# Kernel optimization log

Measured on AMD Instinct MI355X. Metric: run time of the kernel, lower is better.

The kernel has to match this reference:

```python
import jax, jax.numpy as jnp
import numpy as np

B, T, D, H, L, OUT = 512, 82, 129, 1024, 2, 128
TOTAL_LEN = 182  # decoder runs TOTAL_LEN - T = 100 steps


def setup_inputs() -> dict:
    key = jax.random.key(0)
    ks = jax.random.split(key, 32)
    s = 1.0 / np.sqrt(H)  # torch LSTM default init scale
    def p(k, shape):
        return jax.random.uniform(k, shape, dtype=jnp.float32, minval=-s, maxval=s)
    inp = {}
    inp["x"] = jax.random.normal(ks[0], (B, T, D), dtype=jnp.float32)
    inp["lengths"] = jax.random.randint(ks[1], (B,), 1, T + 1, dtype=jnp.int32)
    idx = 2
    for pre, in0 in (("enc", D), ("dec", D - 1)):
        dims = [in0, H]
        for l in range(L):
            inp[f"{pre}_Wih{l}"] = p(ks[idx], (4 * H, dims[l])); idx += 1
            inp[f"{pre}_Whh{l}"] = p(ks[idx], (4 * H, H)); idx += 1
            inp[f"{pre}_bih{l}"] = p(ks[idx], (4 * H,)); idx += 1
            inp[f"{pre}_bhh{l}"] = p(ks[idx], (4 * H,)); idx += 1
    inp["fc_W"] = p(ks[idx], (OUT, H)); idx += 1
    inp["fc_b"] = p(ks[idx], (OUT,))
    return inp


def _cell(x, h, c, Wih, Whh, bih, bhh):
    # torch gate order: i, f, g, o
    g = x @ Wih.T + h @ Whh.T + (bih + bhh)
    i, f, gg, o = jnp.split(g, 4, axis=-1)
    c_new = jax.nn.sigmoid(f) * c + jax.nn.sigmoid(i) * jnp.tanh(gg)
    h_new = jax.nn.sigmoid(o) * jnp.tanh(c_new)
    return h_new, c_new


def _forward(x, lengths, enc, dec, fc_W, fc_b):
    Bsz, Tlen, _ = x.shape
    h0 = jnp.zeros((L, Bsz, H), x.dtype)
    c0 = jnp.zeros((L, Bsz, H), x.dtype)
    xs = jnp.swapaxes(x, 0, 1)  # [T, B, D]
    # packed-sequence semantics: state frozen once t >= lengths[b]
    mask = (jnp.arange(Tlen)[:, None] < lengths[None, :])[..., None]  # [T, B, 1]

    def enc_step(carry, inp):
        h, c = carry
        xt, m = inp
        layer_in = xt
        hs, cs = [], []
        for l in range(L):
            hn, cn = _cell(layer_in, h[l], c[l], *enc[l])
            hn = jnp.where(m, hn, h[l])
            cn = jnp.where(m, cn, c[l])
            hs.append(hn); cs.append(cn)
            layer_in = hn
        return (jnp.stack(hs), jnp.stack(cs)), None

    (h, c), _ = jax.lax.scan(enc_step, (h0, c0), (xs, mask))

    steps = TOTAL_LEN - Tlen
    x0 = jnp.zeros((Bsz, D - 1), x.dtype)

    def dec_step(carry, _):
        h, c, xt = carry
        layer_in = xt
        hs, cs = [], []
        for l in range(L):
            hn, cn = _cell(layer_in, h[l], c[l], *dec[l])
            hs.append(hn); cs.append(cn)
            layer_in = hn
        out = layer_in @ fc_W.T + fc_b  # [B, OUT]
        return (jnp.stack(hs), jnp.stack(cs), out), out

    _, outs = jax.lax.scan(dec_step, (h, c, x0), None, length=steps)
    return jnp.swapaxes(outs, 0, 1)  # [B, steps, OUT]


def reference(x, lengths,
              enc_Wih0, enc_Whh0, enc_bih0, enc_bhh0,
              enc_Wih1, enc_Whh1, enc_bih1, enc_bhh1,
              dec_Wih0, dec_Whh0, dec_bih0, dec_bhh0,
              dec_Wih1, dec_Whh1, dec_bih1, dec_bhh1,
              fc_W, fc_b):
    enc = [(enc_Wih0, enc_Whh0, enc_bih0, enc_bhh0),
           (enc_Wih1, enc_Whh1, enc_bih1, enc_bhh1)]
    dec = [(dec_Wih0, dec_Whh0, dec_bih0, dec_bhh0),
           (dec_Wih1, dec_Whh1, dec_bih1, dec_bhh1)]
    return _forward(x, lengths, enc, dec, fc_W, fc_b)
```

## Files before the change

### kernel.cpp

```cpp
#include <hip/hip_runtime.h>
#include <stdint.h>

#define BB 512
#define TT 82
#define DD 129
#define DXP 192
#define HH 1024
#define G4 4096
#define NOUT 128
#define NSTEPS 100

typedef unsigned short u16;
typedef __attribute__((ext_vector_type(8))) _Float16 f16x8;
typedef __attribute__((ext_vector_type(8))) short short8;
typedef __attribute__((ext_vector_type(4))) float f32x4;

__device__ __forceinline__ u16 f2h(float f) {
  _Float16 h = (_Float16)f;
  return __builtin_bit_cast(u16, h);
}
__device__ __forceinline__ float sigm(float x) { return 1.f / (1.f + __expf(-x)); }
__device__ __forceinline__ float tanhfast(float x) {
  float ax = fabsf(x);
  float e = __expf(2.f * ax);
  float t = 1.f - 2.f / (e + 1.f);
  return copysignf(t, x);
}
__device__ __forceinline__ void glds16(const void* g, void* l) {
  __builtin_amdgcn_global_load_lds((const __attribute__((address_space(1))) void*)g,
                                   (__attribute__((address_space(3))) void*)l, 16, 0, 0);
}

struct GemmP {
  const u16* A0; const u16* W0; const u16* A1; const u16* W1;
  const float* bias; float* cst; u16* hnext;
  int K0, K1, t;
  float* scratch; int mode;
};

template <int FUSE>
__global__ __launch_bounds__(256) void step_gemm(
    GemmP q0, GemmP q1, const int* __restrict__ lengths, float* __restrict__ fout)
{
  const GemmP p = (blockIdx.z == 0) ? q0 : q1;
  __shared__ __align__(16) u16 At[2][64 * 64];
  __shared__ __align__(16) u16 Bt[2][64 * 64];
  const int tid = threadIdx.x;
  const int lane = tid & 63;
  const int w = tid >> 6;
  const int m0 = blockIdx.y * 64;
  const int n0 = blockIdx.x * 64;

  const int nIter0 = p.K0 >> 6;
  const int nIterT = nIter0 + (p.K1 >> 6);

  auto stage = [&](int i, int buf) {
    const u16* A; const u16* W; int K; int kb;
    if (i < nIter0) { A = p.A0; W = p.W0; K = p.K0; kb = i << 6; }
    else            { A = p.A1; W = p.W1; K = p.K1; kb = (i - nIter0) << 6; }
    #pragma unroll
    for (int j = 0; j < 2; ++j) {
      int slot = tid + j * 256;
      int r = slot >> 3, c = slot & 7;
      int g = c ^ (r & 7);
      glds16(A + (size_t)(m0 + r) * K + kb + g * 8,
             &At[buf][(j * 256 + w * 64) * 8]);
    }
    #pragma unroll
    for (int j = 0; j < 2; ++j) {
      int slot = tid + j * 256;
      int r = slot >> 3, c = slot & 7;
      int g = c ^ (r & 7);
      glds16(W + (size_t)(n0 + r) * K + kb + g * 8,
             &Bt[buf][(j * 256 + w * 64) * 8]);
    }
  };

  f32x4 acc[4] = {};

  stage(0, 0);
  for (int i = 0; i < nIterT; ++i) {
    __syncthreads();
    if (i + 1 < nIterT) stage(i + 1, (i + 1) & 1);
    const int buf = i & 1;
    #pragma unroll
    for (int kc = 0; kc < 2; ++kc) {
      f16x8 af, bfr[4];
      const int gch = kc * 4 + (lane >> 4);
      {
        int r = w * 16 + (lane & 15);
        int c = gch ^ (r & 7);
        af = __builtin_bit_cast(f16x8, *(const short8*)&At[buf][(r * 8 + c) * 8]);
      }
      #pragma unroll
      for (int tj = 0; tj < 4; ++tj) {
        int r = tj * 16 + (lane & 15);
        int c = gch ^ (r & 7);
        bfr[tj] = __builtin_bit_cast(f16x8, *(const short8*)&Bt[buf][(r * 8 + c) * 8]);
      }
      #pragma unroll
      for (int tj = 0; tj < 4; ++tj)
        acc[tj] = __builtin_amdgcn_mfma_f32_16x16x32_f16(af, bfr[tj], acc[tj], 0, 0, 0);
    }
  }
  __syncthreads();

  const int col = lane & 15;
  const int rq = (lane >> 4) << 2;

  if (FUSE == 1) {
    const int mb = m0 + w * 16 + rq;
    if (p.mode == 2) {
      #pragma unroll
      for (int tj = 0; tj < 4; ++tj) {
        const int n = n0 + tj * 16 + col;
        #pragma unroll
        for (int r = 0; r < 4; ++r)
          p.scratch[((size_t)(mb + r) << 12) + n] = acc[tj][r];
      }
    } else {
      const int j = blockIdx.x * 16 + col;
      float bv[4];
      #pragma unroll
      for (int tj = 0; tj < 4; ++tj) bv[tj] = p.bias[n0 + tj * 16 + col];
      #pragma unroll
      for (int r = 0; r < 4; ++r) {
        const int m = mb + r;
        const size_t idx = ((size_t)m << 10) + j;
        const bool upd = (p.t < 0) || (p.t < lengths[m]);
        if (upd) {
          float g[4];
          #pragma unroll
          for (int tj = 0; tj < 4; ++tj) g[tj] = acc[tj][r] + bv[tj];
          if (p.mode == 1) {
            #pragma unroll
            for (int tj = 0; tj < 4; ++tj)
              g[tj] += p.scratch[((size_t)m << 12) + n0 + tj * 16 + col];
          }
          float cv = p.cst[idx];
          float cn = sigm(g[1]) * cv + sigm(g[0]) * tanhfast(g[2]);
          float hn = sigm(g[3]) * tanhfast(cn);
          p.cst[idx] = cn;
          p.hnext[idx] = f2h(hn);
        } else {
          p.hnext[idx] = p.A0[idx];
        }
      }
    }
  } else {
    const int mb = m0 + w * 16 + rq;
    #pragma unroll
    for (int tj = 0; tj < 4; ++tj) {
      const int n = n0 + tj * 16 + col;
      const float bv = p.bias[n];
      #pragma unroll
      for (int r = 0; r < 4; ++r) {
        const int m = mb + r;
        const float v = acc[tj][r] + bv;
        if (FUSE == 0) {
          fout[(size_t)m * (NSTEPS * NOUT) + n] = v;
        } else {
          fout[((size_t)(m & (BB - 1)) * NSTEPS + (m >> 9)) * NOUT + n] = v;
        }
      }
    }
  }
}

__global__ void conv_wp(const float* __restrict__ w, u16* __restrict__ wb,
                        int C, int Cp, int R, int perm, int total)
{
  int idx = blockIdx.x * 256 + threadIdx.x;
  if (idx >= total) return;
  int cc = idx % Cp;
  int n = idx / Cp;
  int orig = perm ? (((n >> 4) & 3) * (R >> 2) + (n >> 6) * 16 + (n & 15)) : n;
  wb[idx] = f2h(cc < C ? w[(size_t)orig * C + cc] : 0.f);
}

__global__ void conv_b(const float* __restrict__ b1, const float* __restrict__ b2,
                       float* __restrict__ bp)
{
  int n = blockIdx.x * 256 + threadIdx.x;
  if (n >= G4) return;
  int orig = ((n >> 4) & 3) * HH + (n >> 6) * 16 + (n & 15);
  bp[n] = b1[orig] + b2[orig];
}

__global__ void weff_kernel(const float* __restrict__ wih0, const float* __restrict__ fcW,
                            u16* __restrict__ weffb)
{
  int idx = blockIdx.x * 256 + threadIdx.x;
  int k = idx & (HH - 1);
  int n = idx >> 10;
  int orig = ((n >> 4) & 3) * HH + (n >> 6) * 16 + (n & 15);
  float s = 0.f;
  #pragma unroll 4
  for (int j = 0; j < NOUT; ++j) s += wih0[orig * NOUT + j] * fcW[(size_t)j * HH + k];
  weffb[idx] = f2h(s);
}

__global__ void beff_kernel(const float* __restrict__ bih, const float* __restrict__ bhh,
                            const float* __restrict__ wih0, const float* __restrict__ fcb,
                            float* __restrict__ bp)
{
  int n = blockIdx.x * 256 + threadIdx.x;
  if (n >= G4) return;
  int orig = ((n >> 4) & 3) * HH + (n >> 6) * 16 + (n & 15);
  float s = bih[orig] + bhh[orig];
  #pragma unroll 4
  for (int j = 0; j < NOUT; ++j) s += wih0[orig * NOUT + j] * fcb[j];
  bp[n] = s;
}

__global__ void conv_x(const float* __restrict__ x, u16* __restrict__ xb)
{
  int idx = blockIdx.x * 256 + threadIdx.x;
  if (idx >= TT * BB * DXP) return;
  int k = idx % DXP;
  int tb = idx / DXP;
  int b = tb & (BB - 1);
  int t = tb / BB;
  xb[idx] = f2h(k < DD ? x[((size_t)b * TT + t) * DD + k] : 0.f);
}

extern "C" void kernel_launch(void* const* d_in, const int* in_sizes, int n_in,
                              void* d_out, int out_size, void* d_ws, size_t ws_size,
                              hipStream_t stream) {
  (void)in_sizes; (void)n_in; (void)out_size;
  const float* x     = (const float*)d_in[0];
  const int*   lens  = (const int*)d_in[1];
  const float* eWih0 = (const float*)d_in[2];
  const float* eWhh0 = (const float*)d_in[3];
  const float* ebih0 = (const float*)d_in[4];
  const float* ebhh0 = (const float*)d_in[5];
  const float* eWih1 = (const float*)d_in[6];
  const float* eWhh1 = (const float*)d_in[7];
  const float* ebih1 = (const float*)d_in[8];
  const float* ebhh1 = (const float*)d_in[9];
  const float* dWih0 = (const float*)d_in[10];
  const float* dWhh0 = (const float*)d_in[11];
  const float* dbih0 = (const float*)d_in[12];
  const float* dbhh0 = (const float*)d_in[13];
  const float* dWih1 = (const float*)d_in[14];
  const float* dWhh1 = (const float*)d_in[15];
  const float* dbih1 = (const float*)d_in[16];
  const float* dbhh1 = (const float*)d_in[17];
  const float* fcW   = (const float*)d_in[18];
  const float* fcb   = (const float*)d_in[19];
  float* out = (float*)d_out;

  char* p = (char*)d_ws;
  auto carve = [&](size_t bytes) -> void* {
    void* q = (void*)p;
    p += (bytes + 255) & ~(size_t)255;
    return q;
  };
  u16* eWih0b = (u16*)carve((size_t)G4 * DXP * 2);
  u16* eWhh0b = (u16*)carve((size_t)G4 * HH * 2);
  u16* eWih1b = (u16*)carve((size_t)G4 * HH * 2);
  u16* eWhh1b = (u16*)carve((size_t)G4 * HH * 2);
  u16* Weffb  = (u16*)carve((size_t)G4 * HH * 2);
  u16* dWhh0b = (u16*)carve((size_t)G4 * HH * 2);
  u16* dWih1b = (u16*)carve((size_t)G4 * HH * 2);
  u16* dWhh1b = (u16*)carve((size_t)G4 * HH * 2);
  u16* fcWb   = (u16*)carve((size_t)NOUT * HH * 2);
  float* be0  = (float*)carve((size_t)G4 * 4);
  float* be1  = (float*)carve((size_t)G4 * 4);
  float* beff0= (float*)carve((size_t)G4 * 4);
  float* bd1  = (float*)carve((size_t)G4 * 4);
  u16* xb     = (u16*)carve((size_t)TT * BB * DXP * 2);
  u16* h0p[2] = { (u16*)carve((size_t)BB * HH * 2), (u16*)carve((size_t)BB * HH * 2) };
  u16* h1p[2] = { (u16*)carve((size_t)BB * HH * 2), (u16*)carve((size_t)BB * HH * 2) };
  float* c0   = (float*)carve((size_t)BB * HH * 4);
  float* c1   = (float*)carve((size_t)BB * HH * 4);
  float* scr0 = (float*)carve((size_t)BB * G4 * 4);
  float* scr1 = (float*)carve((size_t)BB * G4 * 4);
  u16* h1hist = (u16*)carve((size_t)(NSTEPS + 1) * BB * HH * 2);
  const size_t need = (size_t)(p - (char*)d_ws);
  const bool bigws = ws_size >= need;

  auto cw = [&](const float* src, u16* dst, int C, int Cp, int R, int perm) {
    int total = R * Cp;
    conv_wp<<<dim3((total + 255) / 256), dim3(256), 0, stream>>>(src, dst, C, Cp, R, perm, total);
  };
  cw(eWih0, eWih0b, DD, DXP, G4, 1);
  cw(eWhh0, eWhh0b, HH, HH, G4, 1);
  cw(eWih1, eWih1b, HH, HH, G4, 1);
  cw(eWhh1, eWhh1b, HH, HH, G4, 1);
  cw(dWhh0, dWhh0b, HH, HH, G4, 1);
  cw(dWih1, dWih1b, HH, HH, G4, 1);
  cw(dWhh1, dWhh1b, HH, HH, G4, 1);
  cw(fcW, fcWb, HH, HH, NOUT, 0);
  weff_kernel<<<dim3(G4 * HH / 256), dim3(256), 0, stream>>>(dWih0, fcW, Weffb);
  conv_b<<<dim3(16), dim3(256), 0, stream>>>(ebih0, ebhh0, be0);
  conv_b<<<dim3(16), dim3(256), 0, stream>>>(ebih1, ebhh1, be1);
  beff_kernel<<<dim3(16), dim3(256), 0, stream>>>(dbih0, dbhh0, dWih0, fcb, beff0);
  conv_b<<<dim3(16), dim3(256), 0, stream>>>(dbih1, dbhh1, bd1);
  conv_x<<<dim3((TT * BB * DXP + 255) / 256), dim3(256), 0, stream>>>(x, xb);

  hipMemsetAsync(h0p[0], 0, (size_t)BB * HH * 2, stream);
  hipMemsetAsync(h1p[0], 0, (size_t)BB * HH * 2, stream);
  hipMemsetAsync(c0, 0, (size_t)BB * HH * 4, stream);
  hipMemsetAsync(c1, 0, (size_t)BB * HH * 4, stream);

  const dim3 g1(64, 8, 1);
  const dim3 g2(64, 8, 2);

  auto L0 = [&](int t) -> GemmP {
    return GemmP{ h0p[t & 1], eWhh0b, xb + (size_t)t * BB * DXP, eWih0b,
                  be0, c0, h0p[(t + 1) & 1], HH, DXP, t, nullptr, 0 };
  };
  auto L1e = [&](int t, u16* dst) -> GemmP {
    return GemmP{ h1p[t & 1], eWhh1b, h0p[(t + 1) & 1], eWih1b,
                  be1, c1, dst, HH, HH, t, nullptr, 0 };
  };

  step_gemm<1><<<g1, 256, 0, stream>>>(L0(0), L0(0), lens, nullptr);
  for (int t = 0; t < TT - 1; ++t)
    step_gemm<1><<<g2, 256, 0, stream>>>(L1e(t, h1p[(t + 1) & 1]), L0(t + 1), lens, nullptr);

  if (bigws) {
    auto hs = [&](int s) { return h1hist + (size_t)s * BB * HH; };
    GemmP pa00{ h0p[0], dWhh0b, nullptr, nullptr, nullptr, nullptr, nullptr,
                HH, 0, -1, scr0, 2 };
    step_gemm<1><<<g2, 256, 0, stream>>>(L1e(TT - 1, hs(0)), pa00, lens, nullptr);

    for (int s = 0; s < NSTEPS; ++s) {
      GemmP d0b{ hs(s), Weffb, nullptr, nullptr, beff0, c0, h0p[(s + 1) & 1],
                 HH, 0, -1, scr0, 1 };
      GemmP d1a{ hs(s), dWhh1b, nullptr, nullptr, nullptr, nullptr, nullptr,
                 HH, 0, -1, scr1, 2 };
      step_gemm<1><<<g2, 256, 0, stream>>>(d0b, d1a, lens, nullptr);

      GemmP d1b{ h0p[(s + 1) & 1], dWih1b, nullptr, nullptr, bd1, c1, hs(s + 1),
                 HH, 0, -1, scr1, 1 };
      if (s + 1 < NSTEPS) {
        GemmP d0a{ h0p[(s + 1) & 1], dWhh0b, nullptr, nullptr, nullptr, nullptr, nullptr,
                   HH, 0, -1, scr0, 2 };
        step_gemm<1><<<g2, 256, 0, stream>>>(d1b, d0a, lens, nullptr);
      } else {
        step_gemm<1><<<g1, 256, 0, stream>>>(d1b, d1b, lens, nullptr);
      }
    }
    GemmP pfc{ hs(1), fcWb, nullptr, nullptr, fcb, nullptr, nullptr, HH, 0, -1,
               nullptr, 0 };
    step_gemm<2><<<dim3(2, (NSTEPS * BB) / 64, 1), 256, 0, stream>>>(pfc, pfc, nullptr, out);
  } else {
    step_gemm<1><<<g1, 256, 0, stream>>>(L1e(TT - 1, h1p[TT & 1]),
                                         L1e(TT - 1, h1p[TT & 1]), lens, nullptr);
    for (int s = 0; s < NSTEPS; ++s) {
      GemmP dl0{ h0p[s & 1], dWhh0b, h1p[s & 1], Weffb,
                 beff0, c0, h0p[(s + 1) & 1], HH, HH, -1, nullptr, 0 };
      step_gemm<1><<<g1, 256, 0, stream>>>(dl0, dl0, lens, nullptr);
      GemmP dl1{ h1p[s & 1], dWhh1b, h0p[(s + 1) & 1], dWih1b,
                 bd1, c1, h1p[(s + 1) & 1], HH, HH, -1, nullptr, 0 };
      step_gemm<1><<<g1, 256, 0, stream>>>(dl1, dl1, lens, nullptr);
      GemmP pfc{ h1p[(s + 1) & 1], fcWb, nullptr, nullptr, fcb, nullptr, nullptr,
                 HH, 0, -1, nullptr, 0 };
      step_gemm<0><<<dim3(2, 8, 1), 256, 0, stream>>>(pfc, pfc, nullptr, out + (size_t)s * NOUT);
    }
  }
}
```

Before: 6.441 ms.

## Split encoder layer-1 input GEMM into its own z-slice and pipeline three stages

In the large-workspace path, the encoder layer-1 input projection (h0 @ Wih1) is now computed as a separate partial GEMM into scratch one step ahead. The per-step launch then runs three independent slices: the layer-1 recurrent GEMM (K=1024 instead of 2048), the next layer-1 input projection, and the next layer-0 step. This shortens the critical-path K for layer 1 and adds parallel blocks per launch, at the cost of extra scratch traffic and a larger grid per launch.

```diff
diff --git a/kernel.cpp b/kernel.cpp
--- a/kernel.cpp
+++ b/kernel.cpp
@@ -40,9 +40,10 @@
 
 template <int FUSE>
 __global__ __launch_bounds__(256) void step_gemm(
-    GemmP q0, GemmP q1, const int* __restrict__ lengths, float* __restrict__ fout)
-{
-  const GemmP p = (blockIdx.z == 0) ? q0 : q1;
+    GemmP q0, GemmP q1, GemmP q2, const int* __restrict__ lengths,
+    float* __restrict__ fout)
+{
+  const GemmP p = (blockIdx.z == 0) ? q0 : ((blockIdx.z == 1) ? q1 : q2);
   __shared__ __align__(16) u16 At[2][64 * 64];
   __shared__ __align__(16) u16 Bt[2][64 * 64];
   const int tid = threadIdx.x;
@@ -306,59 +307,77 @@
 
   const dim3 g1(64, 8, 1);
   const dim3 g2(64, 8, 2);
-
+  const dim3 g3(64, 8, 3);
+
+  float* scrX[2] = { scr0, scr1 };
   auto L0 = [&](int t) -> GemmP {
     return GemmP{ h0p[t & 1], eWhh0b, xb + (size_t)t * BB * DXP, eWih0b,
                   be0, c0, h0p[(t + 1) & 1], HH, DXP, t, nullptr, 0 };
   };
-  auto L1e = [&](int t, u16* dst) -> GemmP {
-    return GemmP{ h1p[t & 1], eWhh1b, h0p[(t + 1) & 1], eWih1b,
-                  be1, c1, dst, HH, HH, t, nullptr, 0 };
-  };
-
-  step_gemm<1><<<g1, 256, 0, stream>>>(L0(0), L0(0), lens, nullptr);
-  for (int t = 0; t < TT - 1; ++t)
-    step_gemm<1><<<g2, 256, 0, stream>>>(L1e(t, h1p[(t + 1) & 1]), L0(t + 1), lens, nullptr);
+  auto XI = [&](int t) -> GemmP {
+    return GemmP{ h0p[(t + 1) & 1], eWih1b, nullptr, nullptr,
+                  nullptr, nullptr, nullptr, HH, 0, -1, scrX[t & 1], 2 };
+  };
+  auto L1C = [&](int t, u16* dst) -> GemmP {
+    return GemmP{ h1p[t & 1], eWhh1b, nullptr, nullptr,
+                  be1, c1, dst, HH, 0, t, scrX[t & 1], 1 };
+  };
 
   if (bigws) {
     auto hs = [&](int s) { return h1hist + (size_t)s * BB * HH; };
+    step_gemm<1><<<g1, 256, 0, stream>>>(L0(0), L0(0), L0(0), lens, nullptr);
+    step_gemm<1><<<g2, 256, 0, stream>>>(XI(0), L0(1), L0(1), lens, nullptr);
+    for (int t = 0; t < TT - 2; ++t)
+      step_gemm<1><<<g3, 256, 0, stream>>>(L1C(t, h1p[(t + 1) & 1]), XI(t + 1), L0(t + 2),
+                                           lens, nullptr);
+    step_gemm<1><<<g2, 256, 0, stream>>>(L1C(TT - 2, h1p[(TT - 1) & 1]), XI(TT - 1),
+                                         XI(TT - 1), lens, nullptr);
     GemmP pa00{ h0p[0], dWhh0b, nullptr, nullptr, nullptr, nullptr, nullptr,
                 HH, 0, -1, scr0, 2 };
-    step_gemm<1><<<g2, 256, 0, stream>>>(L1e(TT - 1, hs(0)), pa00, lens, nullptr);
+    step_gemm<1><<<g2, 256, 0, stream>>>(L1C(TT - 1, hs(0)), pa00, pa00, lens, nullptr);
 
     for (int s = 0; s < NSTEPS; ++s) {
       GemmP d0b{ hs(s), Weffb, nullptr, nullptr, beff0, c0, h0p[(s + 1) & 1],
                  HH, 0, -1, scr0, 1 };
       GemmP d1a{ hs(s), dWhh1b, nullptr, nullptr, nullptr, nullptr, nullptr,
                  HH, 0, -1, scr1, 2 };
-      step_gemm<1><<<g2, 256, 0, stream>>>(d0b, d1a, lens, nullptr);
+      step_gemm<1><<<g2, 256, 0, stream>>>(d0b, d1a, d1a, lens, nullptr);
 
       GemmP d1b{ h0p[(s + 1) & 1], dWih1b, nullptr, nullptr, bd1, c1, hs(s + 1),
                  HH, 0, -1, scr1, 1 };
       if (s + 1 < NSTEPS) {
         GemmP d0a{ h0p[(s + 1) & 1], dWhh0b, nullptr, nullptr, nullptr, nullptr, nullptr,
                    HH, 0, -1, scr0, 2 };
-        step_gemm<1><<<g2, 256, 0, stream>>>(d1b, d0a, lens, nullptr);
+        step_gemm<1><<<g2, 256, 0, stream>>>(d1b, d0a, d0a, lens, nullptr);
       } else {
-        step_gemm<1><<<g1, 256, 0, stream>>>(d1b, d1b, lens, nullptr);
+        step_gemm<1><<<g1, 256, 0, stream>>>(d1b, d1b, d1b, lens, nullptr);
       }
     }
     GemmP pfc{ hs(1), fcWb, nullptr, nullptr, fcb, nullptr, nullptr, HH, 0, -1,
                nullptr, 0 };
-    step_gemm<2><<<dim3(2, (NSTEPS * BB) / 64, 1), 256, 0, stream>>>(pfc, pfc, nullptr, out);
+    step_gemm<2><<<dim3(2, (NSTEPS * BB) / 64, 1), 256, 0, stream>>>(pfc, pfc, pfc, nullptr, out);
   } else {
+    auto L1e = [&](int t, u16* dst) -> GemmP {
+      return GemmP{ h1p[t & 1], eWhh1b, h0p[(t + 1) & 1], eWih1b,
+                    be1, c1, dst, HH, HH, t, nullptr, 0 };
+    };
+    step_gemm<1><<<g1, 256, 0, stream>>>(L0(0), L0(0), L0(0), lens, nullptr);
+    for (int t = 0; t < TT - 1; ++t)
+      step_gemm<1><<<g2, 256, 0, stream>>>(L1e(t, h1p[(t + 1) & 1]), L0(t + 1), L0(t + 1),
+                                           lens, nullptr);
     step_gemm<1><<<g1, 256, 0, stream>>>(L1e(TT - 1, h1p[TT & 1]),
+                                         L1e(TT - 1, h1p[TT & 1]),
                                          L1e(TT - 1, h1p[TT & 1]), lens, nullptr);
     for (int s = 0; s < NSTEPS; ++s) {
       GemmP dl0{ h0p[s & 1], dWhh0b, h1p[s & 1], Weffb,
                  beff0, c0, h0p[(s + 1) & 1], HH, HH, -1, nullptr, 0 };
-      step_gemm<1><<<g1, 256, 0, stream>>>(dl0, dl0, lens, nullptr);
+      step_gemm<1><<<g1, 256, 0, stream>>>(dl0, dl0, dl0, lens, nullptr);
       GemmP dl1{ h1p[s & 1], dWhh1b, h0p[(s + 1) & 1], dWih1b,
                  bd1, c1, h1p[(s + 1) & 1], HH, HH, -1, nullptr, 0 };
-      step_gemm<1><<<g1, 256, 0, stream>>>(dl1, dl1, lens, nullptr);
+      step_gemm<1><<<g1, 256, 0, stream>>>(dl1, dl1, dl1, lens, nullptr);
       GemmP pfc{ h1p[(s + 1) & 1], fcWb, nullptr, nullptr, fcb, nullptr, nullptr,
                  HH, 0, -1, nullptr, 0 };
-      step_gemm<0><<<dim3(2, 8, 1), 256, 0, stream>>>(pfc, pfc, nullptr, out + (size_t)s * NOUT);
+      step_gemm<0><<<dim3(2, 8, 1), 256, 0, stream>>>(pfc, pfc, pfc, nullptr, out + (size_t)s * NOUT);
     }
   }
 }
```

New measurement: 6.765 ms. 5.0% more time.
